# Optimization experiments

Hardware: AMD Instinct MI355X
Metric: run time of the kernel (lower is better)

Reference implementation:

```python
import jax, jax.numpy as jnp
import numpy as np

NUM_LAYERS = 24
LN_EPS = 1e-5


def setup_inputs() -> dict:
    key = jax.random.key(0)
    ks = jax.random.split(key, 8)
    B, S = 256, 8192
    x = jax.random.uniform(ks[0], (B, S, 5), dtype=jnp.float32)
    # per-layer LayerNorm(4) params (torch default init: weight=1, bias=0; use
    # randomized values so the gather is non-trivial)
    ln_w = 1.0 + 0.1 * jax.random.normal(ks[1], (NUM_LAYERS, 4), dtype=jnp.float32)
    ln_b = 0.1 * jax.random.normal(ks[2], (NUM_LAYERS, 4), dtype=jnp.float32)
    # MLP 5 -> 64 -> 32 -> 1 (dropout inactive in eval mode)
    W1 = jax.random.normal(ks[3], (64, 5), dtype=jnp.float32) / np.sqrt(5)
    b1 = jnp.zeros((64,), dtype=jnp.float32)
    W2 = jax.random.normal(ks[4], (32, 64), dtype=jnp.float32) / np.sqrt(64)
    b2 = jnp.zeros((32,), dtype=jnp.float32)
    W3 = jax.random.normal(ks[5], (1, 32), dtype=jnp.float32) / np.sqrt(32)
    b3 = jnp.zeros((1,), dtype=jnp.float32)
    return {"x": x, "ln_w": ln_w, "ln_b": ln_b, "W1": W1, "b1": b1,
            "W2": W2, "b2": b2, "W3": W3, "b3": b3}


def reference(x, ln_w, ln_b, W1, b1, W2, b2, W3, b3):
    B, S, _ = x.shape
    x_flat = x.reshape(-1, 5)                      # [N, 5]
    layer_pos = x_flat[:, -1]                      # [N]
    layer_ids = jnp.clip((layer_pos * NUM_LAYERS).astype(jnp.int32), 0, NUM_LAYERS - 1)
    feats = x_flat[:, :4]                          # [N, 4]
    # vectorized per-token LayerNorm: gather per-token gamma/beta by layer id
    mean = jnp.mean(feats, axis=-1, keepdims=True)
    var = jnp.mean(jnp.square(feats - mean), axis=-1, keepdims=True)  # biased, as torch LN
    normed = (feats - mean) * jax.lax.rsqrt(var + LN_EPS)
    normed = normed * ln_w[layer_ids] + ln_b[layer_ids]               # [N, 4]
    x_norm = jnp.concatenate([normed, layer_pos[:, None]], axis=1)    # [N, 5]
    h = jax.nn.relu(x_norm @ W1.T + b1)            # [N, 64]
    h = jax.nn.relu(h @ W2.T + b2)                 # [N, 32]
    scores = h @ W3.T + b3                         # [N, 1]
    return scores.reshape(B, S)
```

## Files before the change

kernel.cpp:

```cpp
#include <hip/hip_runtime.h>
#include <stdint.h>

#define NUM_LAYERS 24
#define LN_EPS 1e-5f
#define N_ROWS (256 * 8192)
#define NUM_BLOCKS 2048

typedef __attribute__((ext_vector_type(4)))  uint32_t u32x4;
typedef __attribute__((ext_vector_type(16))) float    f32x16;
typedef __attribute__((ext_vector_type(2)))  float    f32x2;
typedef __attribute__((ext_vector_type(2)))  __fp16   h16x2;

__device__ __forceinline__ uint32_t pk_f16_rtz(float lo, float hi) {
    h16x2 v = __builtin_amdgcn_cvt_pkrtz(lo, hi);
    uint32_t u; __builtin_memcpy(&u, &v, 4);
    return u;
}
__device__ __forceinline__ uint32_t pk_f16_rne(float lo, float hi) {
    __fp16 a = (__fp16)lo, b = (__fp16)hi;
    uint16_t ua, ub;
    __builtin_memcpy(&ua, &a, 2); __builtin_memcpy(&ub, &b, 2);
    return (uint32_t)ua | ((uint32_t)ub << 16);
}
__device__ __forceinline__ uint32_t pk_relu_f16(uint32_t d) {
    h16x2 v; __builtin_memcpy(&v, &d, 4);
    h16x2 z = {(__fp16)0.0f, (__fp16)0.0f};
    v = __builtin_elementwise_max(v, z);
    uint32_t u; __builtin_memcpy(&u, &v, 4);
    return u;
}

__device__ __forceinline__ u32x4 make_frag(uint32_t d0, uint32_t d1,
                                           uint32_t d2, uint32_t d3) {
    u32x4 f; f.x = d0; f.y = d1; f.z = d2; f.w = d3;
    return f;
}

__device__ __forceinline__ void mfma_l1(f32x16& d0, f32x16& d1,
                                        const u32x4& a0, const u32x4& a1,
                                        const u32x4& b) {
    asm("s_nop 2\n\t"
        "v_mfma_f32_32x32x16_f16 %0, %2, %4, 0\n\t"
        "v_mfma_f32_32x32x16_f16 %1, %3, %4, 0"
        : "=&v"(d0), "=&v"(d1)
        : "v"(a0), "v"(a1), "v"(b));
}
__device__ __forceinline__ void mfma_l2z(f32x16& c0, f32x16& c1,
                                         const u32x4& w0, const u32x4& w1,
                                         const u32x4& w2, const u32x4& w3,
                                         const u32x4& h00, const u32x4& h01,
                                         const u32x4& h02, const u32x4& h03,
                                         const u32x4& h10, const u32x4& h11,
                                         const u32x4& h12, const u32x4& h13) {
    asm("s_nop 2\n\t"
        "v_mfma_f32_32x32x16_f16 %0, %2, %6, 0\n\t"
        "v_mfma_f32_32x32x16_f16 %1, %2, %10, 0\n\t"
        "v_mfma_f32_32x32x16_f16 %0, %3, %7, %0\n\t"
        "v_mfma_f32_32x32x16_f16 %1, %3, %11, %1\n\t"
        "v_mfma_f32_32x32x16_f16 %0, %4, %8, %0\n\t"
        "v_mfma_f32_32x32x16_f16 %1, %4, %12, %1\n\t"
        "v_mfma_f32_32x32x16_f16 %0, %5, %9, %0\n\t"
        "v_mfma_f32_32x32x16_f16 %1, %5, %13, %1"
        : "=&v"(c0), "=&v"(c1)
        : "v"(w0), "v"(w1), "v"(w2), "v"(w3),
          "v"(h00), "v"(h01), "v"(h02), "v"(h03),
          "v"(h10), "v"(h11), "v"(h12), "v"(h13));
}
__device__ __forceinline__ void mfma_fence2(f32x16& c0, f32x16& c1) {
    asm volatile("s_nop 7\n\ts_nop 7\n\ts_nop 7" : "+v"(c0), "+v"(c1));
}

__device__ __forceinline__ int sigma_k(int p) {
    int hh = (p >> 2) & 1;
    int base = (p & 31) - 4 * hh;
    int r = (base & 3) + 4 * (base >> 3);
    return 32 * (p >> 5) + 16 * (r >> 3) + 8 * hh + (r & 7);
}

__global__ __launch_bounds__(256, 4) void router_mfma(
    const float* __restrict__ x,
    const float* __restrict__ ln_w,
    const float* __restrict__ ln_b,
    const float* __restrict__ W1,
    const float* __restrict__ b1,
    const float* __restrict__ W2,
    const float* __restrict__ b2,
    const float* __restrict__ W3,
    const float* __restrict__ b3,
    float* __restrict__ out)
{
    __shared__ uint32_t s_a1[2 * 64 * 4];
    __shared__ uint32_t s_w2[4 * 64 * 4];
    __shared__ float    s_wb[8 * 64 * 4];
    __shared__ float    s_ln[8 * NUM_LAYERS];

    const int t = threadIdx.x;

    if (t < 8 * NUM_LAYERS) {
        const int q = t & 7, lid = t >> 3;
        s_ln[q * NUM_LAYERS + lid] =
            (q < 4) ? ln_w[lid * 4 + q] : ln_b[lid * 4 + (q - 4)];
    }
    if (t < 128) {
        const int mt = t >> 6, ln = t & 63;
        const int n32l = ln & 31, hl = ln >> 5;
        uint32_t d0 = 0, d1 = 0, d2 = 0;
        if (!hl) {
            const int k = sigma_k(mt * 32 + n32l);
            d0 = pk_f16_rne(W1[k * 5 + 0], W1[k * 5 + 1]);
            d1 = pk_f16_rne(W1[k * 5 + 2], W1[k * 5 + 3]);
            d2 = pk_f16_rne(W1[k * 5 + 4], b1[k]);
        }
        uint32_t* p = &s_a1[(mt * 64 + ln) * 4];
        p[0] = d0; p[1] = d1; p[2] = d2; p[3] = 0;
    }
    {
        const int kt = t >> 6, ln = t & 63;
        const int n32l = ln & 31, hl = ln >> 5;
        const float* wp = W2 + n32l * 64 + kt * 16 + hl * 8;
        const float4 lo = *(const float4*)(wp);
        const float4 hi = *(const float4*)(wp + 4);
        uint32_t* p = &s_w2[(kt * 64 + ln) * 4];
        p[0] = pk_f16_rne(lo.x, lo.y);
        p[1] = pk_f16_rne(lo.z, lo.w);
        p[2] = pk_f16_rne(hi.x, hi.y);
        p[3] = pk_f16_rne(hi.z, hi.w);
    }
#pragma unroll
    for (int e = t; e < 512; e += 256) {
        const int r2 = e >> 6, ln = e & 63;
        const int hl = ln >> 5;
        const int n = ((2 * r2) & 3) + 8 * (r2 >> 1) + 4 * hl;
        float* p = &s_wb[e * 4];
        p[0] = W3[n]; p[1] = W3[n + 1];
        p[2] = b2[n]; p[3] = b2[n + 1];
    }
    __syncthreads();

    const int lane = t & 63;
    const int wid  = t >> 6;
    const int h    = lane >> 5;

    u32x4 a1f[2], w2f[4];
#pragma unroll
    for (int mt = 0; mt < 2; ++mt)
        a1f[mt] = *(const u32x4*)&s_a1[(mt * 64 + lane) * 4];
#pragma unroll
    for (int kt = 0; kt < 4; ++kt)
        w2f[kt] = *(const u32x4*)&s_w2[(kt * 64 + lane) * 4];

    const float b3v = b3[0];
    const f32x2 z2 = {0.0f, 0.0f};

    const int w = blockIdx.x * 4 + wid;
    const size_t rowBase = (size_t)w * 256;

    float4 cv[4];
    float  cl[4];
#pragma unroll
    for (int g = 0; g < 4; ++g) {
        const float* p = x + (rowBase + 64 * g + lane) * 5;
        cv[g] = *(const float4*)p;
        cl[g] = p[4];
    }

#pragma unroll
    for (int g = 0; g < 4; ++g) {
        const size_t gbase = rowBase + 64 * g;

        int lid = (int)(cl[g] * (float)NUM_LAYERS);
        lid = lid < 0 ? 0 : (lid > NUM_LAYERS - 1 ? NUM_LAYERS - 1 : lid);

        const float m  = (cv[g].x + cv[g].y + cv[g].z + cv[g].w) * 0.25f;
        const float d0 = cv[g].x - m, d1 = cv[g].y - m,
                    d2 = cv[g].z - m, d3 = cv[g].w - m;
        const float var = (d0 * d0 + d1 * d1 + d2 * d2 + d3 * d3) * 0.25f;
        const float r   = rsqrtf(var + LN_EPS);

        const float xn0 = fmaf(d0, r * s_ln[0 * 24 + lid], s_ln[4 * 24 + lid]);
        const float xn1 = fmaf(d1, r * s_ln[1 * 24 + lid], s_ln[5 * 24 + lid]);
        const float xn2 = fmaf(d2, r * s_ln[2 * 24 + lid], s_ln[6 * 24 + lid]);
        const float xn3 = fmaf(d3, r * s_ln[3 * 24 + lid], s_ln[7 * 24 + lid]);

        const uint32_t e0 = pk_f16_rtz(xn0, xn1);
        const uint32_t e1 = pk_f16_rtz(xn2, xn3);
        const uint32_t e2 = pk_f16_rtz(cl[g], 1.0f);
        const uint32_t x0 = __shfl_xor((int)e0, 32, 64);
        const uint32_t x1 = __shfl_xor((int)e1, 32, 64);
        const uint32_t x2 = __shfl_xor((int)e2, 32, 64);

        const u32x4 bf_t0 = make_frag(e0, e1, e2, 0u);
        const u32x4 bf_t1 = make_frag(x0, x1, x2, 0u);

        u32x4 h1f0[4], h1f1[4];
        {
            f32x16 c1a, c1b;
            mfma_l1(c1a, c1b, a1f[0], a1f[1], bf_t0);
            mfma_fence2(c1a, c1b);
#pragma unroll
            for (int kt = 0; kt < 4; ++kt) {
                const f32x16& c1 = (kt < 2) ? c1a : c1b;
                const int roff = 8 * (kt & 1);
                uint32_t dw[4];
#pragma unroll
                for (int d = 0; d < 4; ++d)
                    dw[d] = pk_relu_f16(
                        pk_f16_rtz(c1[roff + 2 * d], c1[roff + 2 * d + 1]));
                h1f0[kt] = make_frag(dw[0], dw[1], dw[2], dw[3]);
            }
        }
        {
            f32x16 c1a, c1b;
            mfma_l1(c1a, c1b, a1f[0], a1f[1], bf_t1);
            mfma_fence2(c1a, c1b);
#pragma unroll
            for (int kt = 0; kt < 4; ++kt) {
                const f32x16& c1 = (kt < 2) ? c1a : c1b;
                const int roff = 8 * (kt & 1);
                uint32_t dw[4];
#pragma unroll
                for (int d = 0; d < 4; ++d)
                    dw[d] = pk_relu_f16(
                        pk_f16_rtz(c1[roff + 2 * d], c1[roff + 2 * d + 1]));
                h1f1[kt] = make_frag(dw[0], dw[1], dw[2], dw[3]);
            }
        }

        f32x16 c2_0, c2_1;
        mfma_l2z(c2_0, c2_1,
                 w2f[0], w2f[1], w2f[2], w2f[3],
                 h1f0[0], h1f0[1], h1f0[2], h1f0[3],
                 h1f1[0], h1f1[1], h1f1[2], h1f1[3]);
        mfma_fence2(c2_0, c2_1);

        f32x2 acc0 = z2, acc1 = z2;
#pragma unroll
        for (int r2 = 0; r2 < 8; ++r2) {
            const float4 wb = *(const float4*)&s_wb[(r2 * 64 + lane) * 4];
            f32x2 v0 = {c2_0[2 * r2] + wb.z, c2_0[2 * r2 + 1] + wb.w};
            f32x2 v1 = {c2_1[2 * r2] + wb.z, c2_1[2 * r2 + 1] + wb.w};
            v0 = __builtin_elementwise_max(v0, z2);
            v1 = __builtin_elementwise_max(v1, z2);
            const f32x2 w3v = {wb.x, wb.y};
            acc0 = v0 * w3v + acc0;
            acc1 = v1 * w3v + acc1;
        }
        float q0 = acc0.x + acc0.y;
        float q1 = acc1.x + acc1.y;
        q0 += __shfl_xor(q0, 32, 64);
        q1 += __shfl_xor(q1, 32, 64);

        out[gbase + lane] = (h ? q1 : q0) + b3v;
    }
}

extern "C" void kernel_launch(void* const* d_in, const int* in_sizes, int n_in,
                              void* d_out, int out_size, void* d_ws, size_t ws_size,
                              hipStream_t stream) {
    const float* x    = (const float*)d_in[0];
    const float* ln_w = (const float*)d_in[1];
    const float* ln_b = (const float*)d_in[2];
    const float* W1   = (const float*)d_in[3];
    const float* b1   = (const float*)d_in[4];
    const float* W2   = (const float*)d_in[5];
    const float* b2   = (const float*)d_in[6];
    const float* W3   = (const float*)d_in[7];
    const float* b3   = (const float*)d_in[8];
    float* out = (float*)d_out;

    router_mfma<<<NUM_BLOCKS, 256, 0, stream>>>(x, ln_w, ln_b, W1, b1, W2, b2,
                                                W3, b3, out);
}
```

Measured before the change: 107.0 us.

## Use persistent-style waves with double-buffered row prefetch and higher occupancy

Shrinks the grid so each wave processes 6 or 7 groups of 64 rows, and replaces the upfront load of all groups with a two-slot rolling prefetch that overlaps global loads with MFMA compute. Raises the launch-bounds occupancy target to 5 blocks per CU, splits the layer-2 MFMA chain into two asm blocks, and packs the LayerNorm math into f32x2 operations with a native rsq. The goal is to hide memory latency and reduce register pressure. The uneven per-wave work split and the tighter register budget could cause imbalance or spills.

```diff
diff --git a/kernel.cpp b/kernel.cpp
--- a/kernel.cpp
+++ b/kernel.cpp
@@ -4,11 +4,12 @@
 #define NUM_LAYERS 24
 #define LN_EPS 1e-5f
 #define N_ROWS (256 * 8192)
-#define NUM_BLOCKS 2048
+#define NUM_BLOCKS 1280
 
 typedef __attribute__((ext_vector_type(4)))  uint32_t u32x4;
 typedef __attribute__((ext_vector_type(16))) float    f32x16;
 typedef __attribute__((ext_vector_type(2)))  float    f32x2;
+typedef __attribute__((ext_vector_type(4)))  float    f32x4;
 typedef __attribute__((ext_vector_type(2)))  __fp16   h16x2;
 
 __device__ __forceinline__ uint32_t pk_f16_rtz(float lo, float hi) {
@@ -45,26 +46,29 @@
         : "=&v"(d0), "=&v"(d1)
         : "v"(a0), "v"(a1), "v"(b));
 }
-__device__ __forceinline__ void mfma_l2z(f32x16& c0, f32x16& c1,
+__device__ __forceinline__ void mfma_l2a(f32x16& c0, f32x16& c1,
                                          const u32x4& w0, const u32x4& w1,
+                                         const u32x4& h00, const u32x4& h01,
+                                         const u32x4& h10, const u32x4& h11) {
+    asm("s_nop 2\n\t"
+        "v_mfma_f32_32x32x16_f16 %0, %2, %4, 0\n\t"
+        "v_mfma_f32_32x32x16_f16 %1, %2, %6, 0\n\t"
+        "v_mfma_f32_32x32x16_f16 %0, %3, %5, %0\n\t"
+        "v_mfma_f32_32x32x16_f16 %1, %3, %7, %1"
+        : "=&v"(c0), "=&v"(c1)
+        : "v"(w0), "v"(w1), "v"(h00), "v"(h01), "v"(h10), "v"(h11));
+}
+__device__ __forceinline__ void mfma_l2b(f32x16& c0, f32x16& c1,
                                          const u32x4& w2, const u32x4& w3,
-                                         const u32x4& h00, const u32x4& h01,
                                          const u32x4& h02, const u32x4& h03,
-                                         const u32x4& h10, const u32x4& h11,
                                          const u32x4& h12, const u32x4& h13) {
     asm("s_nop 2\n\t"
-        "v_mfma_f32_32x32x16_f16 %0, %2, %6, 0\n\t"
-        "v_mfma_f32_32x32x16_f16 %1, %2, %10, 0\n\t"
-        "v_mfma_f32_32x32x16_f16 %0, %3, %7, %0\n\t"
-        "v_mfma_f32_32x32x16_f16 %1, %3, %11, %1\n\t"
-        "v_mfma_f32_32x32x16_f16 %0, %4, %8, %0\n\t"
-        "v_mfma_f32_32x32x16_f16 %1, %4, %12, %1\n\t"
-        "v_mfma_f32_32x32x16_f16 %0, %5, %9, %0\n\t"
-        "v_mfma_f32_32x32x16_f16 %1, %5, %13, %1"
-        : "=&v"(c0), "=&v"(c1)
-        : "v"(w0), "v"(w1), "v"(w2), "v"(w3),
-          "v"(h00), "v"(h01), "v"(h02), "v"(h03),
-          "v"(h10), "v"(h11), "v"(h12), "v"(h13));
+        "v_mfma_f32_32x32x16_f16 %0, %2, %4, %0\n\t"
+        "v_mfma_f32_32x32x16_f16 %1, %2, %6, %1\n\t"
+        "v_mfma_f32_32x32x16_f16 %0, %3, %5, %0\n\t"
+        "v_mfma_f32_32x32x16_f16 %1, %3, %7, %1"
+        : "+v"(c0), "+v"(c1)
+        : "v"(w2), "v"(w3), "v"(h02), "v"(h03), "v"(h12), "v"(h13));
 }
 __device__ __forceinline__ void mfma_fence2(f32x16& c0, f32x16& c1) {
     asm volatile("s_nop 7\n\ts_nop 7\n\ts_nop 7" : "+v"(c0), "+v"(c1));
@@ -77,7 +81,7 @@
     return 32 * (p >> 5) + 16 * (r >> 3) + 8 * hh + (r & 7);
 }
 
-__global__ __launch_bounds__(256, 4) void router_mfma(
+__global__ __launch_bounds__(256, 5) void router_mfma(
     const float* __restrict__ x,
     const float* __restrict__ ln_w,
     const float* __restrict__ ln_b,
@@ -92,14 +96,21 @@
     __shared__ uint32_t s_a1[2 * 64 * 4];
     __shared__ uint32_t s_w2[4 * 64 * 4];
     __shared__ float    s_wb[8 * 64 * 4];
-    __shared__ float    s_ln[8 * NUM_LAYERS];
+    __shared__ f32x2    s_lnw[2 * NUM_LAYERS];
+    __shared__ f32x2    s_lnb[2 * NUM_LAYERS];
 
     const int t = threadIdx.x;
 
-    if (t < 8 * NUM_LAYERS) {
-        const int q = t & 7, lid = t >> 3;
-        s_ln[q * NUM_LAYERS + lid] =
-            (q < 4) ? ln_w[lid * 4 + q] : ln_b[lid * 4 + (q - 4)];
+    if (t < 4 * NUM_LAYERS) {
+        const int q2 = t / NUM_LAYERS;
+        const int lid = t % NUM_LAYERS;
+        const int half = q2 & 1;
+        const float* src = (q2 < 2) ? ln_w : ln_b;
+        f32x2 v;
+        v.x = src[lid * 4 + 2 * half];
+        v.y = src[lid * 4 + 2 * half + 1];
+        if (q2 < 2) s_lnw[half * NUM_LAYERS + lid] = v;
+        else        s_lnb[half * NUM_LAYERS + lid] = v;
     }
     if (t < 128) {
         const int mt = t >> 6, ln = t & 63;
@@ -153,38 +164,31 @@
     const f32x2 z2 = {0.0f, 0.0f};
 
     const int w = blockIdx.x * 4 + wid;
-    const size_t rowBase = (size_t)w * 256;
-
-    float4 cv[4];
-    float  cl[4];
-#pragma unroll
-    for (int g = 0; g < 4; ++g) {
-        const float* p = x + (rowBase + 64 * g + lane) * 5;
-        cv[g] = *(const float4*)p;
-        cl[g] = p[4];
-    }
-
-#pragma unroll
-    for (int g = 0; g < 4; ++g) {
-        const size_t gbase = rowBase + 64 * g;
-
-        int lid = (int)(cl[g] * (float)NUM_LAYERS);
+    const bool full7 = (w < 2048);
+    const size_t rowBase =
+        full7 ? (size_t)w * 448 : (size_t)w * 384 + 131072;
+
+    auto body = [&](const f32x4 cv, const float cl, const size_t gbase) {
+        int lid = (int)(cl * (float)NUM_LAYERS);
         lid = lid < 0 ? 0 : (lid > NUM_LAYERS - 1 ? NUM_LAYERS - 1 : lid);
 
-        const float m  = (cv[g].x + cv[g].y + cv[g].z + cv[g].w) * 0.25f;
-        const float d0 = cv[g].x - m, d1 = cv[g].y - m,
-                    d2 = cv[g].z - m, d3 = cv[g].w - m;
-        const float var = (d0 * d0 + d1 * d1 + d2 * d2 + d3 * d3) * 0.25f;
-        const float r   = rsqrtf(var + LN_EPS);
-
-        const float xn0 = fmaf(d0, r * s_ln[0 * 24 + lid], s_ln[4 * 24 + lid]);
-        const float xn1 = fmaf(d1, r * s_ln[1 * 24 + lid], s_ln[5 * 24 + lid]);
-        const float xn2 = fmaf(d2, r * s_ln[2 * 24 + lid], s_ln[6 * 24 + lid]);
-        const float xn3 = fmaf(d3, r * s_ln[3 * 24 + lid], s_ln[7 * 24 + lid]);
-
-        const uint32_t e0 = pk_f16_rtz(xn0, xn1);
-        const uint32_t e1 = pk_f16_rtz(xn2, xn3);
-        const uint32_t e2 = pk_f16_rtz(cl[g], 1.0f);
+        const f32x2 xy = {cv.x, cv.y}, zw = {cv.z, cv.w};
+        const f32x2 s2 = xy + zw;
+        const float m  = (s2.x + s2.y) * 0.25f;
+        const f32x2 m2 = {m, m};
+        const f32x2 d01 = xy - m2, d23 = zw - m2;
+        const f32x2 vv  = d01 * d01 + d23 * d23;
+        const float var = (vv.x + vv.y) * 0.25f;
+        const float r   = __builtin_amdgcn_rsqf(var + LN_EPS);
+        const f32x2 rr  = {r, r};
+        const f32x2 w01 = s_lnw[lid],              w23 = s_lnw[NUM_LAYERS + lid];
+        const f32x2 b01 = s_lnb[lid],              b23 = s_lnb[NUM_LAYERS + lid];
+        const f32x2 xn01 = d01 * (rr * w01) + b01;
+        const f32x2 xn23 = d23 * (rr * w23) + b23;
+
+        const uint32_t e0 = pk_f16_rtz(xn01.x, xn01.y);
+        const uint32_t e1 = pk_f16_rtz(xn23.x, xn23.y);
+        const uint32_t e2 = pk_f16_rtz(cl, 1.0f);
         const uint32_t x0 = __shfl_xor((int)e0, 32, 64);
         const uint32_t x1 = __shfl_xor((int)e1, 32, 64);
         const uint32_t x2 = __shfl_xor((int)e2, 32, 64);
@@ -227,10 +231,10 @@
         }
 
         f32x16 c2_0, c2_1;
-        mfma_l2z(c2_0, c2_1,
-                 w2f[0], w2f[1], w2f[2], w2f[3],
-                 h1f0[0], h1f0[1], h1f0[2], h1f0[3],
-                 h1f1[0], h1f1[1], h1f1[2], h1f1[3]);
+        mfma_l2a(c2_0, c2_1, w2f[0], w2f[1],
+                 h1f0[0], h1f0[1], h1f1[0], h1f1[1]);
+        mfma_l2b(c2_0, c2_1, w2f[2], w2f[3],
+                 h1f0[2], h1f0[3], h1f1[2], h1f1[3]);
         mfma_fence2(c2_0, c2_1);
 
         f32x2 acc0 = z2, acc1 = z2;
@@ -251,7 +255,28 @@
         q1 += __shfl_xor(q1, 32, 64);
 
         out[gbase + lane] = (h ? q1 : q0) + b3v;
-    }
+    };
+
+    f32x4 cvA, cvB;
+    float clA, clB;
+#define PF_A(OFF) do { const float* p = x + (rowBase + (OFF) + lane) * 5; \
+                       cvA = *(const f32x4*)p; clA = p[4]; } while (0)
+#define PF_B(OFF) do { const float* p = x + (rowBase + (OFF) + lane) * 5; \
+                       cvB = *(const f32x4*)p; clB = p[4]; } while (0)
+
+    PF_A(0);
+    PF_B(64);
+    body(cvA, clA, rowBase + 0);    PF_A(128);
+    body(cvB, clB, rowBase + 64);   PF_B(192);
+    body(cvA, clA, rowBase + 128);  PF_A(256);
+    body(cvB, clB, rowBase + 192);  PF_B(320);
+    body(cvA, clA, rowBase + 256);
+    if (full7) PF_A(384);
+    body(cvB, clB, rowBase + 320);
+    if (full7) body(cvA, clA, rowBase + 384);
+
+#undef PF_A
+#undef PF_B
 }
 
 extern "C" void kernel_launch(void* const* d_in, const int* in_sizes, int n_in,
```

Result: slower. 131.1 us (+22.6%).
